# Performance work log

Hardware: AMD Instinct MI355X
Metric: run time of the kernel (lower is better)

The kernel has to match this reference:

```python
import jax, jax.numpy as jnp
import numpy as np
import math

B, N, D, H = 1, 128, 256, 8
DK = D // H

def setup_inputs() -> dict:
    key = jax.random.key(0)
    ks = jax.random.split(key, 8)
    query = jax.random.normal(ks[0], (B, N, N, D), dtype=jnp.float32)
    key_t = jax.random.normal(ks[1], (B, N, N, D), dtype=jnp.float32)
    value = jax.random.normal(ks[2], (B, N, N, D), dtype=jnp.float32)
    mask = jax.random.randint(ks[3], (B, N, N, N), 0, 2).astype(jnp.bool_)
    s = 1.0 / math.sqrt(D)
    # torch nn.Linear weights: [out_features, in_features]
    Wk = jax.random.uniform(ks[4], (D, D), dtype=jnp.float32, minval=-s, maxval=s)
    Wv = jax.random.uniform(ks[5], (D, D), dtype=jnp.float32, minval=-s, maxval=s)
    Wq = jax.random.uniform(ks[6], (D, D), dtype=jnp.float32, minval=-s, maxval=s)
    Wo = jax.random.uniform(ks[7], (D, D), dtype=jnp.float32, minval=-s, maxval=s)
    return {"query": query, "key": key_t, "value": value, "mask": mask,
            "Wq": Wq, "Wk": Wk, "Wv": Wv, "Wo": Wo}

def reference(query, key, value, mask, Wq, Wk, Wv, Wo):
    b, n = query.shape[0], query.shape[1]
    # linear projections (no bias), then split heads -> [b, n, n, h, d_k]
    q = (query @ Wq.T).reshape(b, n, n, H, DK)
    k = (key @ Wk.T).reshape(b, n, n, H, DK)
    v = (value @ Wv.T).reshape(b, n, n, H, DK)
    scale = 1.0 / math.sqrt(DK)
    neg = jnp.float32(-1e9)
    m = mask[..., None]  # [b, n, n, n, 1] broadcast over heads
    # row attention: edge (x,y) attends over edges (x,z)
    scores_r = jnp.einsum('bxyhd,bxzhd->bxyzh', q, k) * scale
    scores_r = jnp.where(m, neg, scores_r)
    # column attention: edge (x,y) attends over edges (z,y)
    scores_l = jnp.einsum('bxyhd,bzyhd->bxyzh', q, k) * scale
    scores_l = jnp.where(m, neg, scores_l)
    scores = jnp.concatenate((scores_r, scores_l), axis=3)  # [b,n,n,2n,h]
    att = jax.nn.softmax(scores, axis=3)
    att_r, att_l = att[:, :, :, :n], att[:, :, :, n:]
    x_r = jnp.einsum('bxyzh,bxzhd->bxyhd', att_r, v)
    x_l = jnp.einsum('bxyzh,bzyhd->bxyhd', att_l, v)
    x = (x_r + x_l).reshape(b, n, n, D)
    return x @ Wo.T
```

## Files before the change

kernel.cpp:

```cpp
#include <hip/hip_runtime.h>
#include <hip/hip_bf16.h>
#include <math.h>

#define N_DIM 128
#define NH 8
#define DKH 32
#define M_ROWS (N_DIM * N_DIM)

typedef __attribute__((ext_vector_type(8))) short bf16x8;
typedef __attribute__((ext_vector_type(4))) float f32x4;

__device__ inline ushort f2b(float x) {
    union { __hip_bfloat16 b; ushort u; } c;
    c.b = __float2bfloat16(x);
    return c.u;
}

#define GLDS(src, dst) \
    __builtin_amdgcn_global_load_lds((const __attribute__((address_space(1))) void*)(src), \
                                     (__attribute__((address_space(3))) void*)(dst), 16, 0, 0)

__global__ __launch_bounds__(256) void prep_kernel(const int* __restrict__ mask,
                                                   ulonglong2* __restrict__ P,
                                                   ulonglong2* __restrict__ PT,
                                                   const float* __restrict__ w0,
                                                   const float* __restrict__ w1,
                                                   const float* __restrict__ w2,
                                                   const float* __restrict__ w3,
                                                   ushort* __restrict__ wout) {
    if (blockIdx.x < 4096) {
        const int row = blockIdx.x * 4 + (threadIdx.x >> 6);
        const int lane = threadIdx.x & 63;
        const int* mrow = mask + (size_t)row * 128;
        unsigned long long lo = __ballot(mrow[lane] != 0);
        unsigned long long hi = __ballot(mrow[64 + lane] != 0);
        if (lane == 0) {
            ulonglong2 v; v.x = lo; v.y = hi;
            P[row] = v;
            PT[(row & 127) * 128 + (row >> 7)] = v;
        }
    } else {
        const int b = blockIdx.x - 4096;
        const int m = b >> 6;
        const float* src = (m == 0) ? w0 : (m == 1) ? w1 : (m == 2) ? w2 : w3;
        const int off = (b & 63) * 1024 + threadIdx.x * 4;
        float4 v = *(const float4*)(src + off);
        union { ushort u[4]; short4 s4; } p;
        p.u[0] = f2b(v.x); p.u[1] = f2b(v.y); p.u[2] = f2b(v.z); p.u[3] = f2b(v.w);
        *(short4*)(wout + (size_t)m * 65536 + off) = p.s4;
    }
}

template <bool AF32, bool OBF16, bool BATCHED>
__global__ __launch_bounds__(256) void gemm3(const void* __restrict__ A0,
                                             const void* __restrict__ A1,
                                             const void* __restrict__ A2,
                                             const ushort* __restrict__ Wbase,
                                             void* __restrict__ Cbase,
                                             float oscale0) {
    __shared__ ushort Ws[128 * 256];
    const int tid = threadIdx.x;
    const int w = tid >> 6, l = tid & 63;
    const int lr = l & 15, g = l >> 4;
    const int row0 = blockIdx.x * 32;
    const int col0 = blockIdx.y * 128;

    const void* Ain = A0;
    const ushort* W = Wbase;
    float oscale = oscale0;
    size_t coff = 0;
    if (BATCHED) {
        const int z = blockIdx.z;
        Ain = (z == 0) ? A0 : (z == 1) ? A1 : A2;
        W += (size_t)z * 65536;
        coff = (size_t)z * ((size_t)M_ROWS * 256);
        oscale = (z == 0) ? oscale0 : 1.0f;
    }

    {
        const int lsub = l >> 5;
        const int lc31 = l & 31;
#pragma unroll
        for (int i = 0; i < 16; i++) {
            const int c2 = w * 16 + i;
            const int r = c2 * 2 + lsub;
            GLDS(W + (size_t)(col0 + r) * 256 + ((lc31 ^ (r & 7)) * 8),
                 &Ws[c2 * 512]);
        }
    }
    __syncthreads();

    const float* Af = (const float*)Ain;
    const ushort* Ab = (const ushort*)Ain;

    f32x4 acc[2][2];
    const f32x4 zero = {0.f, 0.f, 0.f, 0.f};
    acc[0][0] = zero; acc[0][1] = zero; acc[1][0] = zero; acc[1][1] = zero;

#pragma unroll
    for (int ks = 0; ks < 8; ks++) {
        bf16x8 a[2];
#pragma unroll
        for (int fr = 0; fr < 2; fr++) {
            const size_t off = (size_t)(row0 + fr * 16 + lr) * 256 + ks * 32 + g * 8;
            if (AF32) {
                float4 v0 = *(const float4*)(Af + off);
                float4 v1 = *(const float4*)(Af + off + 4);
                union { ushort u[8]; bf16x8 b; } pk;
                pk.u[0] = f2b(v0.x); pk.u[1] = f2b(v0.y);
                pk.u[2] = f2b(v0.z); pk.u[3] = f2b(v0.w);
                pk.u[4] = f2b(v1.x); pk.u[5] = f2b(v1.y);
                pk.u[6] = f2b(v1.z); pk.u[7] = f2b(v1.w);
                a[fr] = pk.b;
            } else {
                a[fr] = *(const bf16x8*)(Ab + off);
            }
        }
#pragma unroll
        for (int fc = 0; fc < 2; fc++) {
            const int rw = w * 32 + fc * 16 + lr;
            bf16x8 b = *(const bf16x8*)((const char*)Ws + rw * 512 +
                                        (((ks * 4 + g) ^ (rw & 7)) * 16));
#pragma unroll
            for (int fr = 0; fr < 2; fr++)
                acc[fr][fc] = __builtin_amdgcn_mfma_f32_16x16x32_bf16(a[fr], b, acc[fr][fc], 0, 0, 0);
        }
    }

#pragma unroll
    for (int fr = 0; fr < 2; fr++)
#pragma unroll
        for (int fc = 0; fc < 2; fc++)
#pragma unroll
            for (int j = 0; j < 4; j++) {
                const int row = row0 + fr * 16 + g * 4 + j;
                const int col = col0 + w * 32 + fc * 16 + lr;
                const float vv = acc[fr][fc][j] * oscale;
                if (OBF16) ((ushort*)Cbase)[coff + (size_t)row * 256 + col] = f2b(vv);
                else       ((float*)Cbase)[(size_t)row * 256 + col] = vv;
            }
}

template <int PASS>
__global__ __launch_bounds__(256) void attn_pass(const ushort* __restrict__ qb,
                                                 const ushort* __restrict__ kb,
                                                 const ushort* __restrict__ vb,
                                                 const ulonglong2* __restrict__ Pm,
                                                 float* __restrict__ ml,
                                                 float* __restrict__ sl,
                                                 float* __restrict__ Pl,
                                                 ushort* __restrict__ xb) {
    __shared__ ushort Ks[128 * 40];
    __shared__ ushort Vt[32 * 128];
    __shared__ ushort Ats[128 * 128];
    __shared__ ulonglong2 Ms[128];

    const int tid = threadIdx.x;
    const int fixed = blockIdx.x >> 3;
    const int h = blockIdx.x & 7;

    int base, stride;
    if (PASS == 0) {
        base = (fixed * NH + h) * DKH;
        stride = N_DIM * NH * DKH;
    } else {
        base = fixed * N_DIM * NH * DKH + h * DKH;
        stride = NH * DKH;
    }

    const int w = tid >> 6;
    const int lane = tid & 63;
    const int lr = lane & 15;
    const int g = lane >> 4;
    const int rbase = w * 32;

    if (tid < 128) Ms[tid] = Pm[fixed * 128 + tid];

    float plv[2][2][4], mlv_r[2][4], slv_r[2][4];
    if (PASS == 1) {
#pragma unroll
        for (int fr = 0; fr < 2; fr++)
#pragma unroll
            for (int j = 0; j < 4; j++) {
                const int row = rbase + fr * 16 + g * 4 + j;
                mlv_r[fr][j] = ml[(size_t)(fixed * NH + h) * N_DIM + row];
                slv_r[fr][j] = sl[(size_t)(fixed * NH + h) * N_DIM + row];
#pragma unroll
                for (int fc = 0; fc < 2; fc++) {
                    const int d = fc * 16 + lr;
                    plv[fr][fc][j] = Pl[((size_t)(fixed * NH + h) * N_DIM + row) * DKH + d];
                }
            }
    }

    bf16x8 aq[2];
#pragma unroll
    for (int fr = 0; fr < 2; fr++)
        aq[fr] = *(const bf16x8*)(qb + (size_t)base +
                                  (size_t)(rbase + fr * 16 + lr) * stride + g * 8);

#pragma unroll
    for (int i = 0; i < 2; i++) {
        int idx = tid + i * 256;
        int r = idx >> 2, d0 = (idx & 3) * 8;
        size_t goff = (size_t)base + (size_t)r * stride + d0;
        int4 kv = *(const int4*)(kb + goff);
        *(int4*)&Ks[r * 40 + d0] = kv;
        union { int4 v4; ushort u[8]; } uu;
        uu.v4 = *(const int4*)(vb + goff);
#pragma unroll
        for (int j = 0; j < 8; j++) {
            int d = d0 + j;
            int byte = d * 256 + r * 2;
            byte ^= (d & 7) << 4;
            Vt[byte >> 1] = uu.u[j];
        }
    }
    __syncthreads();

    f32x4 s[2][8];
    const f32x4 zero = {0.f, 0.f, 0.f, 0.f};
#pragma unroll
    for (int fc = 0; fc < 8; fc++) {
        bf16x8 bk = *(const bf16x8*)&Ks[(fc * 16 + lr) * 40 + g * 8];
#pragma unroll
        for (int fr = 0; fr < 2; fr++)
            s[fr][fc] = __builtin_amdgcn_mfma_f32_16x16x32_bf16(aq[fr], bk, zero, 0, 0, 0);
    }

    float mx[2][4], sm[2][4];
#pragma unroll
    for (int fr = 0; fr < 2; fr++) {
#pragma unroll
        for (int j = 0; j < 4; j++) {
            const int row = rbase + fr * 16 + g * 4 + j;
            const ulonglong2 mb = Ms[row];
            const unsigned long long mls = mb.x >> lr;
            const unsigned long long mhs = mb.y >> lr;
            float mmax = -3.0e38f;
#pragma unroll
            for (int fc = 0; fc < 8; fc++) {
                const int bit = (int)(((fc < 4 ? mls : mhs) >> ((fc & 3) * 16)) & 1ull);
                float val = bit ? -1.0e9f : s[fr][fc][j];
                s[fr][fc][j] = val;
                mmax = fmaxf(mmax, val);
            }
            mmax = fmaxf(mmax, __shfl_xor(mmax, 1));
            mmax = fmaxf(mmax, __shfl_xor(mmax, 2));
            mmax = fmaxf(mmax, __shfl_xor(mmax, 4));
            mmax = fmaxf(mmax, __shfl_xor(mmax, 8));
            float ssum = 0.f;
#pragma unroll
            for (int fc = 0; fc < 8; fc++) {
                const int col = fc * 16 + lr;
                float e = __expf(s[fr][fc][j] - mmax);
                ssum += e;
                int byte = row * 256 + col * 2;
                byte ^= (row & 7) << 4;
                Ats[byte >> 1] = f2b(e);
            }
            ssum += __shfl_xor(ssum, 1);
            ssum += __shfl_xor(ssum, 2);
            ssum += __shfl_xor(ssum, 4);
            ssum += __shfl_xor(ssum, 8);
            mx[fr][j] = mmax;
            sm[fr][j] = ssum;
        }
    }
    __syncthreads();

    f32x4 p[2][2];
    p[0][0] = zero; p[0][1] = zero; p[1][0] = zero; p[1][1] = zero;
#pragma unroll
    for (int ks = 0; ks < 4; ks++) {
        bf16x8 pa[2];
#pragma unroll
        for (int fr = 0; fr < 2; fr++) {
            const int row = rbase + fr * 16 + lr;
            int byte = row * 256 + ks * 64 + g * 16;
            byte ^= (row & 7) << 4;
            pa[fr] = *(const bf16x8*)&Ats[byte >> 1];
        }
#pragma unroll
        for (int fc = 0; fc < 2; fc++) {
            const int rd = fc * 16 + lr;
            int byte = rd * 256 + ks * 64 + g * 16;
            byte ^= (rd & 7) << 4;
            bf16x8 vbf = *(const bf16x8*)&Vt[byte >> 1];
#pragma unroll
            for (int fr = 0; fr < 2; fr++)
                p[fr][fc] = __builtin_amdgcn_mfma_f32_16x16x32_bf16(pa[fr], vbf, p[fr][fc], 0, 0, 0);
        }
    }

    if (PASS == 0) {
#pragma unroll
        for (int fr = 0; fr < 2; fr++) {
#pragma unroll
            for (int j = 0; j < 4; j++) {
                const int row = rbase + fr * 16 + g * 4 + j;
                if (lr == 0) {
                    ml[((size_t)row * NH + h) * N_DIM + fixed] = mx[fr][j];
                    sl[((size_t)row * NH + h) * N_DIM + fixed] = sm[fr][j];
                }
#pragma unroll
                for (int fc = 0; fc < 2; fc++) {
                    const int d = fc * 16 + lr;
                    Pl[((size_t)(row * NH + h) * N_DIM + fixed) * DKH + d] = p[fr][fc][j];
                }
            }
        }
    } else {
#pragma unroll
        for (int fr = 0; fr < 2; fr++) {
#pragma unroll
            for (int j = 0; j < 4; j++) {
                const int row = rbase + fr * 16 + g * 4 + j;
                const float mr = mx[fr][j], sr = sm[fr][j];
                const float mlv = mlv_r[fr][j], slv = slv_r[fr][j];
                const float m = fmaxf(mr, mlv);
                const float cr = __expf(mr - m), cl = __expf(mlv - m);
                const float inv = 1.0f / (sr * cr + slv * cl);
#pragma unroll
                for (int fc = 0; fc < 2; fc++) {
                    const int d = fc * 16 + lr;
                    const float o = (p[fr][fc][j] * cr + plv[fr][fc][j] * cl) * inv;
                    xb[((size_t)fixed * N_DIM + row) * 256 + h * DKH + d] = f2b(o);
                }
            }
        }
    }
}

extern "C" void kernel_launch(void* const* d_in, const int* in_sizes, int n_in,
                              void* d_out, int out_size, void* d_ws, size_t ws_size,
                              hipStream_t stream) {
    const float* query = (const float*)d_in[0];
    const float* key_t = (const float*)d_in[1];
    const float* value = (const float*)d_in[2];
    const int*   mask  = (const int*)d_in[3];
    const float* Wq    = (const float*)d_in[4];
    const float* Wk    = (const float*)d_in[5];
    const float* Wv    = (const float*)d_in[6];
    const float* Wo    = (const float*)d_in[7];

    const size_t MB = 1024 * 1024;
    char* ws = (char*)d_ws;
    ushort*     qb = (ushort*)ws;
    ushort*     kb = qb + (size_t)M_ROWS * 256;
    ushort*     vb = kb + (size_t)M_ROWS * 256;
    ushort*     xb = (ushort*)(ws + 24 * MB);
    float*      Pl = (float*)(ws + 32 * MB);
    float*      ml = (float*)(ws + 48 * MB);
    float*      sl = (float*)(ws + 48 * MB + 512 * 1024);
    ushort*     Wb = (ushort*)(ws + 49 * MB);
    ulonglong2* Pp = (ulonglong2*)(ws + 50 * MB);
    ulonglong2* PT = (ulonglong2*)(ws + 50 * MB + 256 * 1024);

    const float qscale = 0.17677669529663687f;

    prep_kernel<<<4352, 256, 0, stream>>>(mask, Pp, PT, Wq, Wk, Wv, Wo, Wb);
    gemm3<true, true, true><<<dim3(M_ROWS / 32, 2, 3), 256, 0, stream>>>(
        query, key_t, value, Wb, qb, qscale);
    attn_pass<0><<<N_DIM * NH, 256, 0, stream>>>(qb, kb, vb, PT, ml, sl, Pl, xb);
    attn_pass<1><<<N_DIM * NH, 256, 0, stream>>>(qb, kb, vb, Pp, ml, sl, Pl, xb);
    gemm3<false, false, false><<<dim3(M_ROWS / 32, 2, 1), 256, 0, stream>>>(
        xb, nullptr, nullptr, Wb + 3 * 65536, d_out, 1.0f);
}
```

Before: 198.9 us.

## Restructure projection GEMM into 64x256 tiles with double-buffered K-staging

The projection GEMM now computes a full 64x256 output tile per 512-thread block instead of a 32x128 tile, so each A row is read once instead of twice. It streams both A and W through LDS in 32-wide K slices with double buffering and an XOR swizzle, replacing the up-front load of the whole 128x256 weight block. The aim is to cut redundant global A reads and overlap loads with MFMA work. In exchange it adds a barrier per K step, and the A operand for fp32 input is now staged through LDS with a conversion on the store.

Result: faster. 171.2 us (-13.9%).

```diff
diff --git a/kernel.cpp b/kernel.cpp
--- a/kernel.cpp
+++ b/kernel.cpp
@@ -15,6 +15,8 @@
     c.b = __float2bfloat16(x);
     return c.u;
 }
+
+__device__ inline int swz64(int b) { return b ^ (((b >> 7) & 3) << 4); }
 
 #define GLDS(src, dst) \
     __builtin_amdgcn_global_load_lds((const __attribute__((address_space(1))) void*)(src), \
@@ -52,18 +54,19 @@
 }
 
 template <bool AF32, bool OBF16, bool BATCHED>
-__global__ __launch_bounds__(256) void gemm3(const void* __restrict__ A0,
+__global__ __launch_bounds__(512) void gemm5(const void* __restrict__ A0,
                                              const void* __restrict__ A1,
                                              const void* __restrict__ A2,
                                              const ushort* __restrict__ Wbase,
                                              void* __restrict__ Cbase,
                                              float oscale0) {
-    __shared__ ushort Ws[128 * 256];
+    __shared__ ushort As[2][64 * 32];
+    __shared__ ushort Ws[2][256 * 32];
     const int tid = threadIdx.x;
     const int w = tid >> 6, l = tid & 63;
     const int lr = l & 15, g = l >> 4;
-    const int row0 = blockIdx.x * 32;
-    const int col0 = blockIdx.y * 128;
+    const int wm = w & 1, wn = w >> 1;
+    const int row0 = blockIdx.x * 64;
 
     const void* Ain = A0;
     const ushort* W = Wbase;
@@ -77,64 +80,73 @@
         oscale = (z == 0) ? oscale0 : 1.0f;
     }
 
-    {
-        const int lsub = l >> 5;
-        const int lc31 = l & 31;
-#pragma unroll
-        for (int i = 0; i < 16; i++) {
-            const int c2 = w * 16 + i;
-            const int r = c2 * 2 + lsub;
-            GLDS(W + (size_t)(col0 + r) * 256 + ((lc31 ^ (r & 7)) * 8),
-                 &Ws[c2 * 512]);
-        }
-    }
+    auto stage = [&](int t, int buf) {
+        const int kbase = t * 32;
+#pragma unroll
+        for (int i = 0; i < 2; i++) {
+            const int c = w * 2 + i;
+            const int lsw = swz64(c * 1024 + l * 16);
+            GLDS(W + (size_t)(lsw >> 6) * 256 + kbase + ((lsw & 63) >> 1),
+                 &Ws[buf][c * 512]);
+        }
+        if (AF32) {
+            const float* Af = (const float*)Ain;
+            const int rr = tid >> 3, k4 = (tid & 7) * 4;
+            float4 v = *(const float4*)(Af + (size_t)(row0 + rr) * 256 + kbase + k4);
+            union { ushort u[4]; short4 s4; } p;
+            p.u[0] = f2b(v.x); p.u[1] = f2b(v.y); p.u[2] = f2b(v.z); p.u[3] = f2b(v.w);
+            *(short4*)((char*)&As[buf][0] + swz64(rr * 64 + k4 * 2)) = p.s4;
+        } else {
+            if (w < 4) {
+                const ushort* Ab = (const ushort*)Ain;
+                const int lsw = swz64(w * 1024 + l * 16);
+                GLDS(Ab + (size_t)(row0 + (lsw >> 6)) * 256 + kbase + ((lsw & 63) >> 1),
+                     &As[buf][w * 512]);
+            }
+        }
+    };
+
+    f32x4 acc[2][4];
+    const f32x4 zero = {0.f, 0.f, 0.f, 0.f};
+#pragma unroll
+    for (int fr = 0; fr < 2; fr++)
+#pragma unroll
+        for (int fc = 0; fc < 4; fc++) acc[fr][fc] = zero;
+
+    stage(0, 0);
     __syncthreads();
 
-    const float* Af = (const float*)Ain;
-    const ushort* Ab = (const ushort*)Ain;
-
-    f32x4 acc[2][2];
-    const f32x4 zero = {0.f, 0.f, 0.f, 0.f};
-    acc[0][0] = zero; acc[0][1] = zero; acc[1][0] = zero; acc[1][1] = zero;
-
-#pragma unroll
-    for (int ks = 0; ks < 8; ks++) {
-        bf16x8 a[2];
+#pragma unroll
+    for (int t = 0; t < 8; t++) {
+        const int cur = t & 1;
+        if (t < 7) stage(t + 1, cur ^ 1);
+        bf16x8 a[2], bw[4];
 #pragma unroll
         for (int fr = 0; fr < 2; fr++) {
-            const size_t off = (size_t)(row0 + fr * 16 + lr) * 256 + ks * 32 + g * 8;
-            if (AF32) {
-                float4 v0 = *(const float4*)(Af + off);
-                float4 v1 = *(const float4*)(Af + off + 4);
-                union { ushort u[8]; bf16x8 b; } pk;
-                pk.u[0] = f2b(v0.x); pk.u[1] = f2b(v0.y);
-                pk.u[2] = f2b(v0.z); pk.u[3] = f2b(v0.w);
-                pk.u[4] = f2b(v1.x); pk.u[5] = f2b(v1.y);
-                pk.u[6] = f2b(v1.z); pk.u[7] = f2b(v1.w);
-                a[fr] = pk.b;
-            } else {
-                a[fr] = *(const bf16x8*)(Ab + off);
-            }
-        }
-#pragma unroll
-        for (int fc = 0; fc < 2; fc++) {
-            const int rw = w * 32 + fc * 16 + lr;
-            bf16x8 b = *(const bf16x8*)((const char*)Ws + rw * 512 +
-                                        (((ks * 4 + g) ^ (rw & 7)) * 16));
-#pragma unroll
-            for (int fr = 0; fr < 2; fr++)
-                acc[fr][fc] = __builtin_amdgcn_mfma_f32_16x16x32_bf16(a[fr], b, acc[fr][fc], 0, 0, 0);
-        }
+            const int lb = (wm * 32 + fr * 16 + lr) * 64 + g * 16;
+            a[fr] = *(const bf16x8*)((const char*)&As[cur][0] + swz64(lb));
+        }
+#pragma unroll
+        for (int fc = 0; fc < 4; fc++) {
+            const int lb = (wn * 64 + fc * 16 + lr) * 64 + g * 16;
+            bw[fc] = *(const bf16x8*)((const char*)&Ws[cur][0] + swz64(lb));
+        }
+#pragma unroll
+        for (int fr = 0; fr < 2; fr++)
+#pragma unroll
+            for (int fc = 0; fc < 4; fc++)
+                acc[fr][fc] = __builtin_amdgcn_mfma_f32_16x16x32_bf16(a[fr], bw[fc], acc[fr][fc], 0, 0, 0);
+        __syncthreads();
     }
 
 #pragma unroll
     for (int fr = 0; fr < 2; fr++)
 #pragma unroll
-        for (int fc = 0; fc < 2; fc++)
+        for (int fc = 0; fc < 4; fc++)
 #pragma unroll
             for (int j = 0; j < 4; j++) {
-                const int row = row0 + fr * 16 + g * 4 + j;
-                const int col = col0 + w * 32 + fc * 16 + lr;
+                const int row = row0 + wm * 32 + fr * 16 + g * 4 + j;
+                const int col = wn * 64 + fc * 16 + lr;
                 const float vv = acc[fr][fc][j] * oscale;
                 if (OBF16) ((ushort*)Cbase)[coff + (size_t)row * 256 + col] = f2b(vv);
                 else       ((float*)Cbase)[(size_t)row * 256 + col] = vv;
@@ -360,10 +372,10 @@
     const float qscale = 0.17677669529663687f;
 
     prep_kernel<<<4352, 256, 0, stream>>>(mask, Pp, PT, Wq, Wk, Wv, Wo, Wb);
-    gemm3<true, true, true><<<dim3(M_ROWS / 32, 2, 3), 256, 0, stream>>>(
+    gemm5<true, true, true><<<dim3(M_ROWS / 64, 1, 3), 512, 0, stream>>>(
         query, key_t, value, Wb, qb, qscale);
     attn_pass<0><<<N_DIM * NH, 256, 0, stream>>>(qb, kb, vb, PT, ml, sl, Pl, xb);
     attn_pass<1><<<N_DIM * NH, 256, 0, stream>>>(qb, kb, vb, Pp, ml, sl, Pl, xb);
-    gemm3<false, false, false><<<dim3(M_ROWS / 32, 2, 1), 256, 0, stream>>>(
+    gemm5<false, false, false><<<dim3(M_ROWS / 64, 1, 1), 512, 0, stream>>>(
         xb, nullptr, nullptr, Wb + 3 * 65536, d_out, 1.0f);
 }
```
